# Kernel optimization log

Measured on AMD Instinct MI355X. Metric: run time of the kernel, lower is better.

## Reference

```python
import jax, jax.numpy as jnp
import numpy as np

N_NODES = 100000


def _gcn_layer(h, W, b, src, dst, norm, n):
    # h: [N, Fin] -> [N, Fout]; normalized scatter-add aggregation (GCNConv)
    hw = h @ W
    msg = norm[:, None] * hw[src]
    out = jax.ops.segment_sum(msg, dst, num_segments=n)
    return out + b


def setup_inputs() -> dict:
    key = jax.random.key(0)
    k = jax.random.split(key, 10)
    N, E, P, F = N_NODES, 3200000, 500000, 128
    x = jax.random.normal(k[0], (N, F), dtype=jnp.float32)
    edge_index = jax.random.randint(k[1], (2, E), 0, N, dtype=jnp.int64)
    pred_edges = jax.random.randint(k[2], (P, 2), 0, N, dtype=jnp.int64)
    # Glorot-ish init for learned params
    W1 = jax.random.normal(k[3], (F, 16), dtype=jnp.float32) / np.sqrt(F)
    b1 = jnp.zeros((16,), dtype=jnp.float32)
    W2 = jax.random.normal(k[4], (16, 8), dtype=jnp.float32) / np.sqrt(16.0)
    b2 = jnp.zeros((8,), dtype=jnp.float32)
    Wl = jax.random.normal(k[5], (8, 1), dtype=jnp.float32) / np.sqrt(8.0)
    bl = jnp.zeros((1,), dtype=jnp.float32)
    return {"x": x, "edge_index": edge_index, "pred_edges": pred_edges,
            "W1": W1, "b1": b1, "W2": W2, "b2": b2, "Wl": Wl, "bl": bl}


def reference(x, edge_index, pred_edges, W1, b1, W2, b2, Wl, bl):
    n = x.shape[0]
    # GCN norm with self-loops: A_hat = D^{-1/2}(A+I)D^{-1/2}
    loop = jnp.arange(n, dtype=edge_index.dtype)
    src = jnp.concatenate([edge_index[0], loop])
    dst = jnp.concatenate([edge_index[1], loop])
    deg = jax.ops.segment_sum(jnp.ones_like(dst, dtype=x.dtype), dst, num_segments=n)
    dinv = jnp.where(deg > 0, jax.lax.rsqrt(deg), 0.0)
    norm = dinv[src] * dinv[dst]

    h = _gcn_layer(x, W1, b1, src, dst, norm, n)   # [N, 16]
    h = _gcn_layer(h, W2, b2, src, dst, norm, n)   # [N, 8]
    z = jax.nn.sigmoid(h @ Wl + bl)                # [N, 1]
    m = z[pred_edges]                              # [P, 2, 1]
    pred = m[:, 0, 0] * m[:, 1, 0]                 # [P]
    return pred
```

## Files before the change

### kernel.cpp

```cpp
#include <hip/hip_runtime.h>
#include <hip/hip_fp16.h>
#include <math.h>

#define BSHIFT 8
#define BUCK   256
#define TILE   8192
#define CAP    12288

typedef _Float16 f16x4 __attribute__((ext_vector_type(4)));
typedef _Float16 f16x8 __attribute__((ext_vector_type(8)));
typedef float    f32x4 __attribute__((ext_vector_type(4)));


__global__ __launch_bounds__(256) void k_curinit(int* __restrict__ bcursor, int nbuk) {
    int b = blockIdx.x * 256 + threadIdx.x;
    if (b < nbuk) bcursor[b] = b * CAP;
}

__global__ __launch_bounds__(1024) void k_binscatter(const int* __restrict__ src,
                                                     const int* __restrict__ dst,
                                                     int* __restrict__ bcursor,
                                                     int* __restrict__ binned, int E, int nbuk) {
    __shared__ int            payload[TILE];
    __shared__ unsigned short bid16[TILE];
    __shared__ int cnt[512];
    __shared__ int lstart[512];
    __shared__ int gbase[512];
    int t = threadIdx.x;
    int tile0 = blockIdx.x * TILE;
    int tileE = min(TILE, E - tile0);
    if (t < 512) cnt[t] = 0;
    __syncthreads();
    int d[8], s[8];
    int base = t * 8;
    if (base + 8 <= tileE) {
        const int4* d4 = (const int4*)(dst + tile0 + base);
        const int4* s4 = (const int4*)(src + tile0 + base);
        int4 da = d4[0], db = d4[1];
        int4 sa = s4[0], sb = s4[1];
        d[0] = da.x; d[1] = da.y; d[2] = da.z; d[3] = da.w;
        d[4] = db.x; d[5] = db.y; d[6] = db.z; d[7] = db.w;
        s[0] = sa.x; s[1] = sa.y; s[2] = sa.z; s[3] = sa.w;
        s[4] = sb.x; s[5] = sb.y; s[6] = sb.z; s[7] = sb.w;
    } else {
#pragma unroll
        for (int q = 0; q < 8; ++q) {
            int idx = base + q;
            if (idx < tileE) { d[q] = dst[tile0 + idx]; s[q] = src[tile0 + idx]; }
            else d[q] = -1;
        }
    }
#pragma unroll
    for (int q = 0; q < 8; ++q)
        if (d[q] >= 0) atomicAdd(&cnt[d[q] >> BSHIFT], 1);
    __syncthreads();
    if (t < 512) lstart[t] = cnt[t];
    __syncthreads();
    for (int off = 1; off < 512; off <<= 1) {
        int u = (t < 512 && t >= off) ? lstart[t - off] : 0;
        __syncthreads();
        if (t < 512) lstart[t] += u;
        __syncthreads();
    }
    if (t < 512) {
        int c = cnt[t];
        int ex = lstart[t] - c;
        gbase[t] = c ? atomicAdd(&bcursor[t], c) : 0;
        lstart[t] = ex;
        cnt[t] = ex;
    }
    __syncthreads();
#pragma unroll
    for (int q = 0; q < 8; ++q) {
        if (d[q] >= 0) {
            int b = d[q] >> BSHIFT;
            int lp = atomicAdd(&cnt[b], 1);
            payload[lp] = ((d[q] & (BUCK - 1)) << 17) | s[q];
            bid16[lp] = (unsigned short)b;
        }
    }
    __syncthreads();
    for (int k = t; k < tileE; k += 1024) {
        int b = bid16[k];
        int ga = gbase[b] + (k - lstart[b]);
        if (ga < (b + 1) * CAP)
            binned[ga] = payload[k];
    }
}

__global__ __launch_bounds__(1024) void k_sortbucket(const int* __restrict__ bcursor,
                                                     const int* __restrict__ binned,
                                                     int* __restrict__ csr_src,
                                                     int* __restrict__ rowstart,
                                                     int* __restrict__ rowend,
                                                     float* __restrict__ dinv, int N) {
    __shared__ int cnt[BUCK];
    __shared__ int scn[BUCK];
    __shared__ int cur[BUCK];
    int b = blockIdx.x, t = threadIdx.x;
    if (t < BUCK) cnt[t] = 0;
    __syncthreads();
    int beg = b * CAP;
    int end = min(bcursor[b], beg + CAP);
    int v[12];
#pragma unroll
    for (int q = 0; q < 12; ++q) {
        int e = beg + q * 1024 + t;
        v[q] = (e < end) ? binned[e] : -1;
    }
#pragma unroll
    for (int q = 0; q < 12; ++q)
        if (v[q] >= 0) atomicAdd(&cnt[v[q] >> 17], 1);
    __syncthreads();
    if (t < BUCK) scn[t] = cnt[t];
    __syncthreads();
    for (int off = 1; off < BUCK; off <<= 1) {
        int u = (t < BUCK && t >= off) ? scn[t - off] : 0;
        __syncthreads();
        if (t < BUCK) scn[t] += u;
        __syncthreads();
    }
    if (t < BUCK) {
        int excl = scn[t] - cnt[t];
        cur[t] = excl;
        int node = b * BUCK + t;
        if (node < N) {
            rowstart[node] = beg + excl;
            rowend[node]   = beg + scn[t];
            dinv[node] = rsqrtf((float)(cnt[t] + 1));
        }
    }
    __syncthreads();
#pragma unroll
    for (int q = 0; q < 12; ++q) {
        if (v[q] >= 0) {
            int pos = atomicAdd(&cur[v[q] >> 17], 1);
            csr_src[beg + pos] = v[q] & 0x1FFFF;
        }
    }
}


__global__ __launch_bounds__(256) void k_gemm1(const float* __restrict__ x,
                                               const float* __restrict__ W1,
                                               const float* __restrict__ dinv,
                                               __half* __restrict__ hw1h, int N) {
    __shared__ _Float16 sX[64 * 136];
    __shared__ _Float16 sW[16 * 136];
    __shared__ float    sDi[64];
    __shared__ _Float16 sOut[64 * 16];
    int t = threadIdx.x;
    int row0 = blockIdx.x * 64;
    for (int e = t; e < 2048; e += 256) {
        int n = e & 15, k = e >> 4;
        sW[n * 136 + k] = (_Float16)W1[k * 16 + n];
    }
    const float4* x4 = (const float4*)x;
#pragma unroll
    for (int q = 0; q < 8; ++q) {
        int e = q * 256 + t;
        int r = e >> 5, c4 = e & 31;
        int gr = row0 + r;
        float4 v = (gr < N) ? x4[(size_t)gr * 32 + c4] : make_float4(0.f, 0.f, 0.f, 0.f);
        f16x4 hv = {(_Float16)v.x, (_Float16)v.y, (_Float16)v.z, (_Float16)v.w};
        *(f16x4*)&sX[r * 136 + c4 * 4] = hv;
    }
    if (t < 64) sDi[t] = (row0 + t < N) ? dinv[row0 + t] : 0.f;
    __syncthreads();
    int w = t >> 6, l = t & 63;
    int m = l & 15, quad = l >> 4;
    f32x4 acc = {0.f, 0.f, 0.f, 0.f};
#pragma unroll
    for (int kc = 0; kc < 4; ++kc) {
        f16x8 a = *(const f16x8*)&sX[(w * 16 + m) * 136 + kc * 32 + quad * 8];
        f16x8 b = *(const f16x8*)&sW[m * 136 + kc * 32 + quad * 8];
        acc = __builtin_amdgcn_mfma_f32_16x16x32_f16(a, b, acc, 0, 0, 0);
    }
#pragma unroll
    for (int r = 0; r < 4; ++r) {
        int nl = w * 16 + quad * 4 + r;
        sOut[nl * 16 + m] = (_Float16)(acc[r] * sDi[nl]);
    }
    __syncthreads();
    int nn = t >> 2, ch = t & 3;
    int gn = row0 + nn;
    if (gn < N)
        *(float2*)&hw1h[(size_t)gn * 16 + ch * 4] = *(float2*)&sOut[nn * 16 + ch * 4];
}

__global__ __launch_bounds__(256) void k_agg1c(const int* __restrict__ rowstart,
                                               const int* __restrict__ rowend,
                                               const int* __restrict__ csr_src,
                                               const float* __restrict__ dinv,
                                               const f16x8* __restrict__ hw1v,
                                               const float* __restrict__ W2,
                                               const float* __restrict__ b1,
                                               __half* __restrict__ hw2h, int N) {
    __shared__ float sW[128], sb[16];
    __shared__ float sh[128][17];
    __shared__ float sdi[128];
    int t = threadIdx.x;
    if (t < 128) sW[t] = W2[t];
    if (t < 16)  sb[t] = b1[t];
    __syncthreads();
    int g = t >> 1, j = t & 1;
    int i = blockIdx.x * 128 + g;
    float a[8] = {0, 0, 0, 0, 0, 0, 0, 0};
    float di = 0.f;
    if (i < N) {
        int beg = rowstart[i], end = rowend[i];
        di = dinv[i];
        int c0 = beg;
        for (; c0 + 8 <= end; c0 += 8) {
            int sidx[4];
#pragma unroll
            for (int k = 0; k < 4; ++k) sidx[k] = csr_src[c0 + j + 2 * k];
            int sv[8];
#pragma unroll
            for (int m = 0; m < 8; ++m) sv[m] = __shfl(sidx[m >> 1], m & 1, 2);
            f16x8 gv[8];
#pragma unroll
            for (int m = 0; m < 8; ++m) gv[m] = hw1v[2 * (size_t)sv[m] + j];
#pragma unroll
            for (int m = 0; m < 8; ++m)
#pragma unroll
                for (int d = 0; d < 8; ++d) a[d] += (float)gv[m][d];
        }
        for (; c0 < end; ++c0) {
            f16x8 gv = hw1v[2 * (size_t)csr_src[c0] + j];
#pragma unroll
            for (int d = 0; d < 8; ++d) a[d] += (float)gv[d];
        }
        f16x8 self = hw1v[2 * (size_t)i + j];
#pragma unroll
        for (int d = 0; d < 8; ++d)
            a[d] = di * (a[d] + (float)self[d]) + sb[8 * j + d];
    }
#pragma unroll
    for (int d = 0; d < 8; ++d) sh[g][8 * j + d] = a[d];
    if (j == 0) sdi[g] = di;
    __syncthreads();
    if (i < N) {
        int jb = j * 4;
        float o0 = 0.f, o1 = 0.f, o2 = 0.f, o3 = 0.f;
#pragma unroll
        for (int k = 0; k < 16; ++k) {
            float hv = sh[g][k];
            o0 += hv * sW[k * 8 + jb + 0];
            o1 += hv * sW[k * 8 + jb + 1];
            o2 += hv * sW[k * 8 + jb + 2];
            o3 += hv * sW[k * 8 + jb + 3];
        }
        float dd = sdi[g];
        f16x4 hout = {(_Float16)(dd * o0), (_Float16)(dd * o1),
                      (_Float16)(dd * o2), (_Float16)(dd * o3)};
        *(f16x4*)&hw2h[(size_t)i * 8 + jb] = hout;
    }
}

__global__ __launch_bounds__(256) void k_agg2c(const int* __restrict__ rowstart,
                                               const int* __restrict__ rowend,
                                               const int* __restrict__ csr_src,
                                               const float* __restrict__ dinv,
                                               const f16x4* __restrict__ hw2v,
                                               const float* __restrict__ Wl,
                                               const float* __restrict__ b2,
                                               const float* __restrict__ bl,
                                               float* __restrict__ z, int N) {
    __shared__ float sW[8], sb[8], sbl;
    int t = threadIdx.x;
    if (t < 8) { sW[t] = Wl[t]; sb[t] = b2[t]; }
    if (t == 0) sbl = bl[0];
    __syncthreads();
    int g = t >> 1, j = t & 1;
    int i = blockIdx.x * 128 + g;
    float v = 0.f;
    if (i < N) {
        int beg = rowstart[i], end = rowend[i];
        float di = dinv[i];
        float a[4] = {0, 0, 0, 0};
        int c0 = beg;
        for (; c0 + 8 <= end; c0 += 8) {
            int sidx[4];
#pragma unroll
            for (int k = 0; k < 4; ++k) sidx[k] = csr_src[c0 + j + 2 * k];
            int sv[8];
#pragma unroll
            for (int m = 0; m < 8; ++m) sv[m] = __shfl(sidx[m >> 1], m & 1, 2);
            f16x4 gv[8];
#pragma unroll
            for (int m = 0; m < 8; ++m) gv[m] = hw2v[2 * (size_t)sv[m] + j];
#pragma unroll
            for (int m = 0; m < 8; ++m)
#pragma unroll
                for (int d = 0; d < 4; ++d) a[d] += (float)gv[m][d];
        }
        for (; c0 < end; ++c0) {
            f16x4 gv = hw2v[2 * (size_t)csr_src[c0] + j];
#pragma unroll
            for (int d = 0; d < 4; ++d) a[d] += (float)gv[d];
        }
        f16x4 self = hw2v[2 * (size_t)i + j];
#pragma unroll
        for (int d = 0; d < 4; ++d) {
            float h = di * (a[d] + (float)self[d]) + sb[4 * j + d];
            v += h * sW[4 * j + d];
        }
    }
    v += __shfl_xor(v, 1);
    if (i < N && j == 0) z[i] = 1.f / (1.f + __expf(-(v + sbl)));
}

__global__ __launch_bounds__(256) void k_pred(const int2* __restrict__ pe2,
                                              const float* __restrict__ z,
                                              float* __restrict__ out, int P) {
    int p = blockIdx.x * 256 + threadIdx.x;
    if (p < P) {
        int2 e = pe2[p];
        out[p] = z[e.x] * z[e.y];
    }
}


extern "C" void kernel_launch(void* const* d_in, const int* in_sizes, int n_in,
                              void* d_out, int out_size, void* d_ws, size_t ws_size,
                              hipStream_t stream) {
    const float* x  = (const float*)d_in[0];
    const int*   ei = (const int*)d_in[1];
    const int*   pe = (const int*)d_in[2];
    const float* W1 = (const float*)d_in[3];
    const float* b1 = (const float*)d_in[4];
    const float* W2 = (const float*)d_in[5];
    const float* b2 = (const float*)d_in[6];
    const float* Wl = (const float*)d_in[7];
    const float* bl = (const float*)d_in[8];
    float* out = (float*)d_out;

    const int N = in_sizes[0] / 128;
    const int E = in_sizes[1] / 2;
    const int P = in_sizes[2] / 2;
    const int NBUK = (N + BUCK - 1) >> BSHIFT;

    const int* src = ei;
    const int* dst = ei + E;

    float*  ws   = (float*)d_ws;
    float*  dinv = ws;
    __half* hw1h = (__half*)(ws + (size_t)N);
    __half* hw2h = (__half*)(ws + (size_t)9 * N);
    float*  z    = ws + (size_t)13 * N;
    int* rowstart = (int*)(ws + (size_t)14 * N);
    int* rowend   = rowstart + N;
    int* bcursor  = rowend + N;
    int* binned   = bcursor + 512;
    int* csr_src  = binned + (size_t)NBUK * CAP;

    const int B = 256;

    k_curinit<<<(NBUK + B - 1) / B, B, 0, stream>>>(bcursor, NBUK);
    k_binscatter<<<(E + TILE - 1) / TILE, 1024, 0, stream>>>(src, dst, bcursor, binned, E, NBUK);
    k_sortbucket<<<NBUK, 1024, 0, stream>>>(bcursor, binned, csr_src, rowstart, rowend, dinv, N);
    k_gemm1<<<(N + 63) / 64, B, 0, stream>>>(x, W1, dinv, hw1h, N);
    k_agg1c<<<(N + 127) / 128, B, 0, stream>>>(rowstart, rowend, csr_src, dinv,
                                               (const f16x8*)hw1h, W2, b1, hw2h, N);
    k_agg2c<<<(N + 127) / 128, B, 0, stream>>>(rowstart, rowend, csr_src, dinv,
                                               (const f16x4*)hw2h, Wl, b2, bl, z, N);
    k_pred<<<(P + B - 1) / B, B, 0, stream>>>((const int2*)pe, z, out, P);
}
```

Baseline: 215.9 us.

## Use wave-shuffle scans and one-thread-per-node aggregation with recomputed dinv

```diff
diff --git a/kernel.cpp b/kernel.cpp
--- a/kernel.cpp
+++ b/kernel.cpp
@@ -26,6 +26,7 @@
     __shared__ int cnt[512];
     __shared__ int lstart[512];
     __shared__ int gbase[512];
+    __shared__ int wsum[8];
     int t = threadIdx.x;
     int tile0 = blockIdx.x * TILE;
     int tileE = min(TILE, E - tile0);
@@ -54,17 +55,27 @@
     for (int q = 0; q < 8; ++q)
         if (d[q] >= 0) atomicAdd(&cnt[d[q] >> BSHIFT], 1);
     __syncthreads();
-    if (t < 512) lstart[t] = cnt[t];
-    __syncthreads();
-    for (int off = 1; off < 512; off <<= 1) {
-        int u = (t < 512 && t >= off) ? lstart[t - off] : 0;
-        __syncthreads();
-        if (t < 512) lstart[t] += u;
-        __syncthreads();
-    }
+    int c = 0, ex = 0;
     if (t < 512) {
-        int c = cnt[t];
-        int ex = lstart[t] - c;
+        c = cnt[t];
+        int v = c;
+#pragma unroll
+        for (int off = 1; off < 64; off <<= 1) {
+            int u = __shfl_up(v, off, 64);
+            if ((t & 63) >= off) v += u;
+        }
+        if ((t & 63) == 63) wsum[t >> 6] = v;
+        ex = v - c;
+    }
+    __syncthreads();
+    if (t == 0) {
+        int run = 0;
+#pragma unroll
+        for (int w = 0; w < 8; ++w) { int u = wsum[w]; wsum[w] = run; run += u; }
+    }
+    __syncthreads();
+    if (t < 512) {
+        ex += wsum[t >> 6];
         gbase[t] = c ? atomicAdd(&bcursor[t], c) : 0;
         lstart[t] = ex;
         cnt[t] = ex;
@@ -95,8 +106,8 @@
                                                      int* __restrict__ rowend,
                                                      float* __restrict__ dinv, int N) {
     __shared__ int cnt[BUCK];
-    __shared__ int scn[BUCK];
     __shared__ int cur[BUCK];
+    __shared__ int wsum[4];
     int b = blockIdx.x, t = threadIdx.x;
     if (t < BUCK) cnt[t] = 0;
     __syncthreads();
@@ -112,22 +123,33 @@
     for (int q = 0; q < 12; ++q)
         if (v[q] >= 0) atomicAdd(&cnt[v[q] >> 17], 1);
     __syncthreads();
-    if (t < BUCK) scn[t] = cnt[t];
-    __syncthreads();
-    for (int off = 1; off < BUCK; off <<= 1) {
-        int u = (t < BUCK && t >= off) ? scn[t - off] : 0;
-        __syncthreads();
-        if (t < BUCK) scn[t] += u;
-        __syncthreads();
-    }
+    int c = 0, ex = 0;
     if (t < BUCK) {
-        int excl = scn[t] - cnt[t];
-        cur[t] = excl;
+        c = cnt[t];
+        int s = c;
+#pragma unroll
+        for (int off = 1; off < 64; off <<= 1) {
+            int u = __shfl_up(s, off, 64);
+            if ((t & 63) >= off) s += u;
+        }
+        if ((t & 63) == 63) wsum[t >> 6] = s;
+        ex = s - c;
+    }
+    __syncthreads();
+    if (t == 0) {
+        int run = 0;
+#pragma unroll
+        for (int w = 0; w < 4; ++w) { int u = wsum[w]; wsum[w] = run; run += u; }
+    }
+    __syncthreads();
+    if (t < BUCK) {
+        ex += wsum[t >> 6];
+        cur[t] = ex;
         int node = b * BUCK + t;
         if (node < N) {
-            rowstart[node] = beg + excl;
-            rowend[node]   = beg + scn[t];
-            dinv[node] = rsqrtf((float)(cnt[t] + 1));
+            rowstart[node] = beg + ex;
+            rowend[node]   = beg + ex + c;
+            dinv[node] = rsqrtf((float)(c + 1));
         }
     }
     __syncthreads();
@@ -191,78 +213,83 @@
 __global__ __launch_bounds__(256) void k_agg1c(const int* __restrict__ rowstart,
                                                const int* __restrict__ rowend,
                                                const int* __restrict__ csr_src,
-                                               const float* __restrict__ dinv,
                                                const f16x8* __restrict__ hw1v,
                                                const float* __restrict__ W2,
                                                const float* __restrict__ b1,
                                                __half* __restrict__ hw2h, int N) {
     __shared__ float sW[128], sb[16];
-    __shared__ float sh[128][17];
-    __shared__ float sdi[128];
     int t = threadIdx.x;
     if (t < 128) sW[t] = W2[t];
     if (t < 16)  sb[t] = b1[t];
     __syncthreads();
-    int g = t >> 1, j = t & 1;
-    int i = blockIdx.x * 128 + g;
-    float a[8] = {0, 0, 0, 0, 0, 0, 0, 0};
-    float di = 0.f;
-    if (i < N) {
-        int beg = rowstart[i], end = rowend[i];
-        di = dinv[i];
-        int c0 = beg;
-        for (; c0 + 8 <= end; c0 += 8) {
-            int sidx[4];
-#pragma unroll
-            for (int k = 0; k < 4; ++k) sidx[k] = csr_src[c0 + j + 2 * k];
-            int sv[8];
-#pragma unroll
-            for (int m = 0; m < 8; ++m) sv[m] = __shfl(sidx[m >> 1], m & 1, 2);
-            f16x8 gv[8];
-#pragma unroll
-            for (int m = 0; m < 8; ++m) gv[m] = hw1v[2 * (size_t)sv[m] + j];
-#pragma unroll
-            for (int m = 0; m < 8; ++m)
-#pragma unroll
-                for (int d = 0; d < 8; ++d) a[d] += (float)gv[m][d];
-        }
-        for (; c0 < end; ++c0) {
-            f16x8 gv = hw1v[2 * (size_t)csr_src[c0] + j];
-#pragma unroll
-            for (int d = 0; d < 8; ++d) a[d] += (float)gv[d];
-        }
-        f16x8 self = hw1v[2 * (size_t)i + j];
-#pragma unroll
-        for (int d = 0; d < 8; ++d)
-            a[d] = di * (a[d] + (float)self[d]) + sb[8 * j + d];
-    }
-#pragma unroll
-    for (int d = 0; d < 8; ++d) sh[g][8 * j + d] = a[d];
-    if (j == 0) sdi[g] = di;
-    __syncthreads();
-    if (i < N) {
-        int jb = j * 4;
-        float o0 = 0.f, o1 = 0.f, o2 = 0.f, o3 = 0.f;
-#pragma unroll
-        for (int k = 0; k < 16; ++k) {
-            float hv = sh[g][k];
-            o0 += hv * sW[k * 8 + jb + 0];
-            o1 += hv * sW[k * 8 + jb + 1];
-            o2 += hv * sW[k * 8 + jb + 2];
-            o3 += hv * sW[k * 8 + jb + 3];
-        }
-        float dd = sdi[g];
-        f16x4 hout = {(_Float16)(dd * o0), (_Float16)(dd * o1),
-                      (_Float16)(dd * o2), (_Float16)(dd * o3)};
-        *(f16x4*)&hw2h[(size_t)i * 8 + jb] = hout;
-    }
+    int i = blockIdx.x * 256 + t;
+    if (i >= N) return;
+    int beg = rowstart[i], end = rowend[i];
+    float di = rsqrtf((float)(end - beg + 1));
+    float a[16];
+#pragma unroll
+    for (int d = 0; d < 16; ++d) a[d] = 0.f;
+    int c0 = beg;
+    for (; c0 + 8 <= end; c0 += 8) {
+        int s[8];
+#pragma unroll
+        for (int m = 0; m < 8; ++m) s[m] = csr_src[c0 + m];
+        f16x8 lo[8], hi[8];
+#pragma unroll
+        for (int m = 0; m < 8; ++m) {
+            lo[m] = hw1v[2 * (size_t)s[m]];
+            hi[m] = hw1v[2 * (size_t)s[m] + 1];
+        }
+#pragma unroll
+        for (int m = 0; m < 8; ++m) {
+#pragma unroll
+            for (int d = 0; d < 8; ++d) {
+                a[d]     += (float)lo[m][d];
+                a[8 + d] += (float)hi[m][d];
+            }
+        }
+    }
+    for (; c0 < end; ++c0) {
+        int s = csr_src[c0];
+        f16x8 lo = hw1v[2 * (size_t)s];
+        f16x8 hi = hw1v[2 * (size_t)s + 1];
+#pragma unroll
+        for (int d = 0; d < 8; ++d) {
+            a[d]     += (float)lo[d];
+            a[8 + d] += (float)hi[d];
+        }
+    }
+    {
+        f16x8 lo = hw1v[2 * (size_t)i];
+        f16x8 hi = hw1v[2 * (size_t)i + 1];
+#pragma unroll
+        for (int d = 0; d < 8; ++d) {
+            a[d]     += (float)lo[d];
+            a[8 + d] += (float)hi[d];
+        }
+    }
+    float h[16];
+#pragma unroll
+    for (int k = 0; k < 16; ++k) h[k] = di * a[k] + sb[k];
+    float o[8];
+#pragma unroll
+    for (int d = 0; d < 8; ++d) o[d] = 0.f;
+#pragma unroll
+    for (int k = 0; k < 16; ++k) {
+        float hv = h[k];
+#pragma unroll
+        for (int d = 0; d < 8; ++d) o[d] += hv * sW[k * 8 + d];
+    }
+    f16x8 ho;
+#pragma unroll
+    for (int d = 0; d < 8; ++d) ho[d] = (_Float16)(di * o[d]);
+    *(f16x8*)&hw2h[(size_t)i * 8] = ho;
 }
 
 __global__ __launch_bounds__(256) void k_agg2c(const int* __restrict__ rowstart,
                                                const int* __restrict__ rowend,
                                                const int* __restrict__ csr_src,
-                                               const float* __restrict__ dinv,
-                                               const f16x4* __restrict__ hw2v,
+                                               const f16x8* __restrict__ hw2v,
                                                const float* __restrict__ Wl,
                                                const float* __restrict__ b2,
                                                const float* __restrict__ bl,
@@ -272,43 +299,39 @@
     if (t < 8) { sW[t] = Wl[t]; sb[t] = b2[t]; }
     if (t == 0) sbl = bl[0];
     __syncthreads();
-    int g = t >> 1, j = t & 1;
-    int i = blockIdx.x * 128 + g;
+    int i = blockIdx.x * 256 + t;
+    if (i >= N) return;
+    int beg = rowstart[i], end = rowend[i];
+    float di = rsqrtf((float)(end - beg + 1));
+    float a[8];
+#pragma unroll
+    for (int d = 0; d < 8; ++d) a[d] = 0.f;
+    int c0 = beg;
+    for (; c0 + 8 <= end; c0 += 8) {
+        int s[8];
+#pragma unroll
+        for (int m = 0; m < 8; ++m) s[m] = csr_src[c0 + m];
+        f16x8 gv[8];
+#pragma unroll
+        for (int m = 0; m < 8; ++m) gv[m] = hw2v[(size_t)s[m]];
+#pragma unroll
+        for (int m = 0; m < 8; ++m)
+#pragma unroll
+            for (int d = 0; d < 8; ++d) a[d] += (float)gv[m][d];
+    }
+    for (; c0 < end; ++c0) {
+        f16x8 gv = hw2v[(size_t)csr_src[c0]];
+#pragma unroll
+        for (int d = 0; d < 8; ++d) a[d] += (float)gv[d];
+    }
+    f16x8 self = hw2v[(size_t)i];
     float v = 0.f;
-    if (i < N) {
-        int beg = rowstart[i], end = rowend[i];
-        float di = dinv[i];
-        float a[4] = {0, 0, 0, 0};
-        int c0 = beg;
-        for (; c0 + 8 <= end; c0 += 8) {
-            int sidx[4];
-#pragma unroll
-            for (int k = 0; k < 4; ++k) sidx[k] = csr_src[c0 + j + 2 * k];
-            int sv[8];
-#pragma unroll
-            for (int m = 0; m < 8; ++m) sv[m] = __shfl(sidx[m >> 1], m & 1, 2);
-            f16x4 gv[8];
-#pragma unroll
-            for (int m = 0; m < 8; ++m) gv[m] = hw2v[2 * (size_t)sv[m] + j];
-#pragma unroll
-            for (int m = 0; m < 8; ++m)
-#pragma unroll
-                for (int d = 0; d < 4; ++d) a[d] += (float)gv[m][d];
-        }
-        for (; c0 < end; ++c0) {
-            f16x4 gv = hw2v[2 * (size_t)csr_src[c0] + j];
-#pragma unroll
-            for (int d = 0; d < 4; ++d) a[d] += (float)gv[d];
-        }
-        f16x4 self = hw2v[2 * (size_t)i + j];
-#pragma unroll
-        for (int d = 0; d < 4; ++d) {
-            float h = di * (a[d] + (float)self[d]) + sb[4 * j + d];
-            v += h * sW[4 * j + d];
-        }
-    }
-    v += __shfl_xor(v, 1);
-    if (i < N && j == 0) z[i] = 1.f / (1.f + __expf(-(v + sbl)));
+#pragma unroll
+    for (int d = 0; d < 8; ++d) {
+        float h = di * (a[d] + (float)self[d]) + sb[d];
+        v += h * sW[d];
+    }
+    z[i] = 1.f / (1.f + __expf(-(v + sbl)));
 }
 
 __global__ __launch_bounds__(256) void k_pred(const int2* __restrict__ pe2,
@@ -361,9 +384,9 @@
     k_binscatter<<<(E + TILE - 1) / TILE, 1024, 0, stream>>>(src, dst, bcursor, binned, E, NBUK);
     k_sortbucket<<<NBUK, 1024, 0, stream>>>(bcursor, binned, csr_src, rowstart, rowend, dinv, N);
     k_gemm1<<<(N + 63) / 64, B, 0, stream>>>(x, W1, dinv, hw1h, N);
-    k_agg1c<<<(N + 127) / 128, B, 0, stream>>>(rowstart, rowend, csr_src, dinv,
+    k_agg1c<<<(N + 255) / 256, B, 0, stream>>>(rowstart, rowend, csr_src,
                                                (const f16x8*)hw1h, W2, b1, hw2h, N);
-    k_agg2c<<<(N + 127) / 128, B, 0, stream>>>(rowstart, rowend, csr_src, dinv,
-                                               (const f16x4*)hw2h, Wl, b2, bl, z, N);
+    k_agg2c<<<(N + 255) / 256, B, 0, stream>>>(rowstart, rowend, csr_src,
+                                               (const f16x8*)hw2h, Wl, b2, bl, z, N);
     k_pred<<<(P + B - 1) / B, B, 0, stream>>>((const int2*)pe, z, out, P);
 }
```

Measured after the change: 224.3 us. 1.04x slower.
